# Performance work log

Measured on AMD Instinct MI355X. Metric: run time of the kernel, lower is better.

## Reference

```python
import jax, jax.numpy as jnp
import numpy as np

N_NODES = 100000
N_EDGES = 3200000
N_F = 128
HIDDEN = 128
N_PRED = 8
K_HOPS = 3
N_GRAPHS = 64


def setup_inputs() -> dict:
    key = jax.random.key(0)
    k1, k2, k3, k4, k5, k6, k7, k8 = jax.random.split(key, 8)
    x = jax.random.normal(k1, (N_NODES, N_F), dtype=jnp.float32)
    edge_index = jax.random.randint(k2, (2, N_EDGES), 0, N_NODES, dtype=jnp.int64)
    edge_attr = jax.random.uniform(k3, (N_EDGES,), dtype=jnp.float32)
    batch = jnp.sort(jax.random.randint(k4, (N_NODES,), 0, N_GRAPHS, dtype=jnp.int64))
    # SGConv internal Linear: in=n_f, out=hidden (applied after K propagations)
    s1 = 1.0 / np.sqrt(N_F)
    W_conv = jax.random.uniform(k5, (HIDDEN, N_F), dtype=jnp.float32, minval=-s1, maxval=s1)
    b_conv = jax.random.uniform(k6, (HIDDEN,), dtype=jnp.float32, minval=-s1, maxval=s1)
    s2 = 1.0 / np.sqrt(HIDDEN)
    W_lin = jax.random.uniform(k7, (N_PRED, HIDDEN), dtype=jnp.float32, minval=-s2, maxval=s2)
    b_lin = jax.random.uniform(k8, (N_PRED,), dtype=jnp.float32, minval=-s2, maxval=s2)
    return {"x": x, "edge_index": edge_index, "edge_attr": edge_attr, "batch": batch,
            "W_conv": W_conv, "b_conv": b_conv, "W_lin": W_lin, "b_lin": b_lin}


def _gcn_norm(edge_index, edge_weight, num_nodes):
    # Add self-loops with weight 1 (PyG gcn_norm default), then symmetric normalize.
    loop = jnp.arange(num_nodes, dtype=edge_index.dtype)
    row = jnp.concatenate([edge_index[0], loop])
    col = jnp.concatenate([edge_index[1], loop])
    w = jnp.concatenate([edge_weight, jnp.ones((num_nodes,), dtype=edge_weight.dtype)])
    deg = jax.ops.segment_sum(w, col, num_segments=num_nodes)
    dinv = jnp.where(deg > 0, jax.lax.rsqrt(jnp.where(deg > 0, deg, 1.0)), 0.0)
    norm = dinv[row] * w * dinv[col]
    return row, col, norm


def reference(x, edge_index, edge_attr, batch, W_conv, b_conv, W_lin, b_lin):
    N = x.shape[0]
    row, col, norm = _gcn_norm(edge_index, edge_attr, N)
    h = x
    for _ in range(K_HOPS):  # K repeated gather-scale-scatter propagations
        h = jax.ops.segment_sum(norm[:, None] * h[row], col, num_segments=N)
    h = h @ W_conv.T + b_conv  # SGConv linear: [N, hidden]
    # global_mean_pool by batch id
    sums = jax.ops.segment_sum(h, batch, num_segments=N_GRAPHS)
    cnt = jax.ops.segment_sum(jnp.ones((N,), dtype=h.dtype), batch, num_segments=N_GRAPHS)
    pooled = sums / jnp.maximum(cnt, 1.0)[:, None]
    # dropout(p=0.5) is identity in eval mode
    return pooled @ W_lin.T + b_lin
```

## Files before the change

kernel.cpp:

```cpp
#include <hip/hip_runtime.h>

#define NN 100000
#define NE 3200000
#define NF 128
#define NH 128
#define NP 8
#define NG 64

#define CS 16000
#define NC 7
#define NW 64
#define ES (NE / NW)

#define PT 64
#define GP 1024

#define SCAN_B 1024
#define SCAN_NBLK 98

__device__ __forceinline__ unsigned short f2bf(float f) {
    unsigned u = __float_as_uint(f);
    return (unsigned short)((u + 0x7fffu + ((u >> 16) & 1u)) >> 16);
}
__device__ __forceinline__ float bf2f(unsigned short b) {
    return __uint_as_float((unsigned)b << 16);
}

__global__ void k_init(float* __restrict__ cnt, float* __restrict__ psum) {
    int i = blockIdx.x * blockDim.x + threadIdx.x;
    if (i < NG) cnt[i] = 0.0f;
    if (i < NG * NH) psum[i] = 0.0f;
}

__global__ __launch_bounds__(256) void k_hist(const int* __restrict__ row,
                                              unsigned* __restrict__ H) {
    __shared__ unsigned hist[CS];
    int w = blockIdx.x % NW, c = blockIdx.x / NW;
    int rbase = c * CS;
    int nb = (rbase + CS <= NN) ? CS : (NN - rbase);
    for (int i = threadIdx.x; i < nb; i += 256) hist[i] = 0u;
    __syncthreads();
    const int4* r4 = (const int4*)(row + (size_t)w * ES);
    for (int i = threadIdx.x; i < ES / 8; i += 256) {
        int4 a = r4[2 * i], b = r4[2 * i + 1];
        int rs[8] = {a.x, a.y, a.z, a.w, b.x, b.y, b.z, b.w};
#pragma unroll
        for (int j = 0; j < 8; ++j) {
            unsigned rr = (unsigned)(rs[j] - rbase);
            if (rr < (unsigned)nb) atomicAdd(&hist[rr], 1u);
        }
    }
    __syncthreads();
    for (int i = threadIdx.x; i < nb; i += 256) H[(size_t)w * NN + rbase + i] = hist[i];
}

__global__ __launch_bounds__(256) void k_deg_hist(const int* __restrict__ col,
                                                  const float* __restrict__ wt,
                                                  float* __restrict__ Hd) {
    __shared__ float dh[CS];
    int w = blockIdx.x % NW, c = blockIdx.x / NW;
    int rbase = c * CS;
    int nb = (rbase + CS <= NN) ? CS : (NN - rbase);
    for (int i = threadIdx.x; i < nb; i += 256) dh[i] = 0.0f;
    __syncthreads();
    const int4*   c4 = (const int4*)(col + (size_t)w * ES);
    const float4* w4 = (const float4*)(wt + (size_t)w * ES);
    for (int i = threadIdx.x; i < ES / 8; i += 256) {
        int4 a = c4[2 * i], b = c4[2 * i + 1];
        float4 wa = w4[2 * i], wb = w4[2 * i + 1];
        int cc[8] = {a.x, a.y, a.z, a.w, b.x, b.y, b.z, b.w};
        float ww[8] = {wa.x, wa.y, wa.z, wa.w, wb.x, wb.y, wb.z, wb.w};
#pragma unroll
        for (int j = 0; j < 8; ++j) {
            unsigned rr = (unsigned)(cc[j] - rbase);
            if (rr < (unsigned)nb) atomicAdd(&dh[rr], ww[j]);
        }
    }
    __syncthreads();
    for (int i = threadIdx.x; i < nb; i += 256) Hd[(size_t)w * NN + rbase + i] = dh[i];
}

__global__ void k_cnt(const int* __restrict__ batch, float* __restrict__ cnt) {
    __shared__ float c[NG];
    int t = threadIdx.x;
    if (t < NG) c[t] = 0.0f;
    __syncthreads();
    int i = blockIdx.x * blockDim.x + t;
    if (i < NN) atomicAdd(&c[batch[i]], 1.0f);
    __syncthreads();
    if (t < NG && c[t] != 0.0f) atomicAdd(&cnt[t], c[t]);
}

__global__ void k_reduce(const unsigned* __restrict__ H, const float* __restrict__ Hd,
                         int* __restrict__ rcnt, float* __restrict__ dinv) {
    int r = blockIdx.x * blockDim.x + threadIdx.x;
    if (r >= NN) return;
    unsigned s = 0;
    float d = 1.0f;
#pragma unroll
    for (int w = 0; w < NW; ++w) {
        s += H[(size_t)w * NN + r];
        d += Hd[(size_t)w * NN + r];
    }
    rcnt[r] = (int)s;
    dinv[r] = rsqrtf(d);
}

__global__ __launch_bounds__(SCAN_B) void k_scan1(const int* __restrict__ rcnt,
                                                  int* __restrict__ px,
                                                  int* __restrict__ bsum) {
    __shared__ int s[SCAN_B];
    int t = threadIdx.x;
    int i = blockIdx.x * SCAN_B + t;
    int v = (i < NN) ? rcnt[i] : 0;
    s[t] = v;
    __syncthreads();
    for (int off = 1; off < SCAN_B; off <<= 1) {
        int x = (t >= off) ? s[t - off] : 0;
        __syncthreads();
        s[t] += x;
        __syncthreads();
    }
    px[i] = s[t] - v;
    if (t == SCAN_B - 1) bsum[blockIdx.x] = s[t];
}

__global__ void k_scan2(const int* __restrict__ bsum, int* __restrict__ bofs) {
    if (threadIdx.x == 0) {
        int acc = 0;
        for (int b = 0; b < SCAN_NBLK; ++b) { bofs[b] = acc; acc += bsum[b]; }
    }
}

__global__ void k_scan3(const int* __restrict__ px, const int* __restrict__ bofs,
                        int* __restrict__ rowptr) {
    int i = blockIdx.x * blockDim.x + threadIdx.x;
    if (i > NN) return;
    rowptr[i] = px[i] + bofs[i >> 10];
}

__global__ void k_base(const int* __restrict__ rowptr, unsigned* __restrict__ H) {
    int r = blockIdx.x * blockDim.x + threadIdx.x;
    if (r >= NN) return;
    unsigned acc = (unsigned)rowptr[r];
#pragma unroll
    for (int w = 0; w < NW; ++w) {
        unsigned v = H[(size_t)w * NN + r];
        H[(size_t)w * NN + r] = acc;
        acc += v;
    }
}

__global__ __launch_bounds__(256) void k_sort(const int* __restrict__ row,
                                              const int* __restrict__ col,
                                              const float* __restrict__ wt,
                                              const unsigned* __restrict__ B,
                                              const float* __restrict__ dinv,
                                              float2* __restrict__ pack) {
    __shared__ unsigned basel[CS];
    int w = blockIdx.x % NW, c = blockIdx.x / NW;
    int rbase = c * CS;
    int nb = (rbase + CS <= NN) ? CS : (NN - rbase);
    for (int i = threadIdx.x; i < nb; i += 256)
        basel[i] = B[(size_t)w * NN + rbase + i];
    __syncthreads();
    const int4*   r4 = (const int4*)(row + (size_t)w * ES);
    const int4*   c4 = (const int4*)(col + (size_t)w * ES);
    const float4* w4 = (const float4*)(wt + (size_t)w * ES);
    for (int i = threadIdx.x; i < ES / 8; i += 256) {
        int4 ra = r4[2 * i], rb = r4[2 * i + 1];
        int4 ca = c4[2 * i], cb = c4[2 * i + 1];
        float4 wa = w4[2 * i], wb = w4[2 * i + 1];
        int rs[8] = {ra.x, ra.y, ra.z, ra.w, rb.x, rb.y, rb.z, rb.w};
        int cs[8] = {ca.x, ca.y, ca.z, ca.w, cb.x, cb.y, cb.z, cb.w};
        float ww[8] = {wa.x, wa.y, wa.z, wa.w, wb.x, wb.y, wb.z, wb.w};
#pragma unroll
        for (int j = 0; j < 8; ++j) {
            unsigned rr = (unsigned)(rs[j] - rbase);
            if (rr < (unsigned)nb) {
                unsigned pos = atomicAdd(&basel[rr], 1u);
                pack[pos] = make_float2(__int_as_float(cs[j]),
                                        dinv[rs[j]] * ww[j] * dinv[cs[j]]);
            }
        }
    }
}

__global__ void k_q1_gather(const int* __restrict__ rowptr, const float2* __restrict__ pack,
                            const int* __restrict__ batch, const float* __restrict__ dinv,
                            unsigned short* __restrict__ Q) {
    int wid = (blockIdx.x * blockDim.x + threadIdx.x) >> 6;
    int lane = threadIdx.x & 63;
    if (wid >= NN) return;
    int beg = rowptr[wid], end = rowptr[wid + 1];
    float d = dinv[wid];
    float acc = (batch[wid] == lane) ? d * d : 0.0f;
    int e = beg;
    for (; e + 8 <= end; e += 8) {
        float2 p[8];
#pragma unroll
        for (int j = 0; j < 8; ++j) p[j] = pack[e + j];
        int b[8];
#pragma unroll
        for (int j = 0; j < 8; ++j) b[j] = batch[__float_as_int(p[j].x)];
#pragma unroll
        for (int j = 0; j < 8; ++j) acc += (b[j] == lane) ? p[j].y : 0.0f;
    }
    for (; e < end; ++e) {
        float2 p = pack[e];
        acc += (batch[__float_as_int(p.x)] == lane) ? p.y : 0.0f;
    }
    Q[(wid << 6) + lane] = f2bf(acc);
}

__global__ void k_hop_gather(const int* __restrict__ rowptr, const float2* __restrict__ pack,
                             const float* __restrict__ dinv,
                             const unsigned short* __restrict__ Qin,
                             unsigned short* __restrict__ Qout) {
    int wid = (blockIdx.x * blockDim.x + threadIdx.x) >> 6;
    int lane = threadIdx.x & 63;
    if (wid >= NN) return;
    int beg = rowptr[wid], end = rowptr[wid + 1];
    float d = dinv[wid];
    float acc = d * d * bf2f(Qin[(wid << 6) + lane]);
    int e = beg;
    for (; e + 8 <= end; e += 8) {
        float2 p[8];
#pragma unroll
        for (int j = 0; j < 8; ++j) p[j] = pack[e + j];
        unsigned short q[8];
#pragma unroll
        for (int j = 0; j < 8; ++j) q[j] = Qin[(__float_as_int(p[j].x) << 6) + lane];
#pragma unroll
        for (int j = 0; j < 8; ++j) acc += p[j].y * bf2f(q[j]);
    }
    for (; e < end; ++e) {
        float2 p = pack[e];
        acc += p.y * bf2f(Qin[(__float_as_int(p.x) << 6) + lane]);
    }
    Qout[(wid << 6) + lane] = f2bf(acc);
}

__global__ __launch_bounds__(256) void k_pool(const unsigned short* __restrict__ Q,
                                              const float* __restrict__ x,
                                              float* __restrict__ partial) {
    __shared__ unsigned short qsh[PT * NG];
    __shared__ float xs[PT * NF];
    int t = threadIdx.x;
    int f4 = (t & 31) << 2;
    int g0 = (t >> 5) << 3;
    float4 acc[8];
#pragma unroll
    for (int i = 0; i < 8; ++i) acc[i] = make_float4(0.f, 0.f, 0.f, 0.f);

    const int NT = (NN + PT - 1) / PT;
    for (int tile = blockIdx.x; tile < NT; tile += GP) {
        int n0 = tile * PT;
        int nt = min(PT, NN - n0);
        const uint4*  Q4 = (const uint4*)(Q + (size_t)n0 * NG);
        const float4* X4 = (const float4*)(x + (size_t)n0 * NF);
        uint4*  qs4 = (uint4*)qsh;
        float4* xs4 = (float4*)xs;
        for (int i = t; i < nt * (NG / 8); i += 256) qs4[i] = Q4[i];
        for (int i = t; i < nt * (NF / 4); i += 256) xs4[i] = X4[i];
        __syncthreads();
        for (int n = 0; n < nt; ++n) {
            float4 xv = *(const float4*)&xs[n * NF + f4];
            uint4 qu = *(const uint4*)&qsh[n * NG + g0];
            float qv[8];
            qv[0] = __uint_as_float(qu.x << 16);
            qv[1] = __uint_as_float(qu.x & 0xffff0000u);
            qv[2] = __uint_as_float(qu.y << 16);
            qv[3] = __uint_as_float(qu.y & 0xffff0000u);
            qv[4] = __uint_as_float(qu.z << 16);
            qv[5] = __uint_as_float(qu.z & 0xffff0000u);
            qv[6] = __uint_as_float(qu.w << 16);
            qv[7] = __uint_as_float(qu.w & 0xffff0000u);
#pragma unroll
            for (int i = 0; i < 8; ++i) {
                acc[i].x += qv[i] * xv.x;
                acc[i].y += qv[i] * xv.y;
                acc[i].z += qv[i] * xv.z;
                acc[i].w += qv[i] * xv.w;
            }
        }
        __syncthreads();
    }
    float* pb = partial + (size_t)blockIdx.x * (NG * NF);
#pragma unroll
    for (int i = 0; i < 8; ++i)
        *(float4*)&pb[(g0 + i) * NF + f4] = acc[i];
}

__global__ void k_red(const float* __restrict__ partial, float* __restrict__ psum) {
    int gid = blockIdx.x * blockDim.x + threadIdx.x;
    int idx = gid & (NG * NF - 1);
    int j = gid >> 13;
    float acc = 0.0f;
    for (int b = j; b < GP; b += 8)
        acc += partial[(size_t)b * (NG * NF) + idx];
    atomicAdd(&psum[idx], acc);
}

__global__ void k_final(const float* __restrict__ psum, const float* __restrict__ cnt,
                        const float* __restrict__ Wc, const float* __restrict__ bc,
                        const float* __restrict__ Wl, const float* __restrict__ bl,
                        float* __restrict__ out) {
    __shared__ float M[NP * NH];
    __shared__ float bias[NP];
    int t = threadIdx.x;
    for (int idx = t; idx < NP * NH; idx += 256) {
        int p = idx >> 7, f = idx & 127;
        float s = 0.0f;
        for (int h = 0; h < NH; ++h) s += Wl[p * NH + h] * Wc[h * NF + f];
        M[idx] = s;
    }
    if (t < NP) {
        float s = bl[t];
        for (int h = 0; h < NH; ++h) s += Wl[t * NH + h] * bc[h];
        bias[t] = s;
    }
    __syncthreads();
    for (int idx = t; idx < NG * NP; idx += 256) {
        int g = idx >> 3, p = idx & 7;
        float inv = 1.0f / fmaxf(cnt[g], 1.0f);
        float s = 0.0f;
        for (int f = 0; f < NF; ++f) s += psum[g * NF + f] * M[p * NH + f];
        out[idx] = s * inv + bias[p];
    }
}

extern "C" void kernel_launch(void* const* d_in, const int* in_sizes, int n_in,
                              void* d_out, int out_size, void* d_ws, size_t ws_size,
                              hipStream_t stream) {
    const float* x     = (const float*)d_in[0];
    const int*   ei    = (const int*)d_in[1];
    const float* ea    = (const float*)d_in[2];
    const int*   batch = (const int*)d_in[3];
    const float* Wc    = (const float*)d_in[4];
    const float* bc    = (const float*)d_in[5];
    const float* Wl    = (const float*)d_in[6];
    const float* bl    = (const float*)d_in[7];
    const int* row = ei;
    const int* col = ei + NE;
    float* out = (float*)d_out;

    float* ws     = (float*)d_ws;
    float*  dinv   = ws;
    int*    rowptr = (int*)(dinv + NN);
    float*  cnt    = (float*)(rowptr + NN + 4);
    float*  psum   = cnt + NG;
    float2* pack   = (float2*)(psum + NG * NH);
    unsigned* H    = (unsigned*)(pack + NE);
    float*    Hd   = (float*)(H + (size_t)NW * NN);
    unsigned short* Qa = (unsigned short*)H;
    unsigned short* Qb = Qa + (size_t)NN * NG;
    float* partial = (float*)Qb;
    int* rcnt = (int*)pack;
    int* px   = rcnt + SCAN_NBLK * SCAN_B;
    int* bsum = px + SCAN_NBLK * SCAN_B;
    int* bofs = bsum + SCAN_NBLK;

    const int B = 256;
    int gN  = (NN + B - 1) / B;
    int gCW = NC * NW;
    int gW  = (int)(((long long)NN * 64 + B - 1) / B);

    k_init<<<(NG * NH + B - 1) / B, B, 0, stream>>>(cnt, psum);
    k_hist<<<gCW, B, 0, stream>>>(row, H);
    k_deg_hist<<<gCW, B, 0, stream>>>(col, ea, Hd);
    k_cnt<<<gN, B, 0, stream>>>(batch, cnt);
    k_reduce<<<gN, B, 0, stream>>>(H, Hd, rcnt, dinv);

    k_scan1<<<SCAN_NBLK, SCAN_B, 0, stream>>>(rcnt, px, bsum);
    k_scan2<<<1, 64, 0, stream>>>(bsum, bofs);
    k_scan3<<<(NN + 1 + SCAN_B - 1) / SCAN_B, SCAN_B, 0, stream>>>(px, bofs, rowptr);
    k_base<<<gN, B, 0, stream>>>(rowptr, H);
    k_sort<<<gCW, B, 0, stream>>>(row, col, ea, H, dinv, pack);

    k_q1_gather<<<gW, B, 0, stream>>>(rowptr, pack, batch, dinv, Qa);
    k_hop_gather<<<gW, B, 0, stream>>>(rowptr, pack, dinv, Qa, Qb);
    k_hop_gather<<<gW, B, 0, stream>>>(rowptr, pack, dinv, Qb, Qa);

    k_pool<<<GP, B, 0, stream>>>(Qa, x, partial);
    k_red<<<256, B, 0, stream>>>(partial, psum);
    k_final<<<1, B, 0, stream>>>(psum, cnt, Wc, bc, Wl, bl, out);
}
```

Before: 685.8 us.

## Split each wavefront into 8 edge slots with 16-byte bf16 row loads

The gather kernels now split each 64-lane wavefront into 8 edge slots of 8 lanes. Each lane loads a uint4 holding 8 bf16 values of the 64-wide Q row, so each pass handles 8 edges at once. A one-step prefetch of the packed edge data overlaps the next edge load with the current gather. Partial sums are combined with xor shuffles and written as a vectorized uint4 store. This is meant to raise memory-level parallelism and cut per-edge instruction and latency cost, in exchange for more registers and the shuffle reduction.

```diff
diff --git a/kernel.cpp b/kernel.cpp
--- a/kernel.cpp
+++ b/kernel.cpp
@@ -192,25 +192,44 @@
     int wid = (blockIdx.x * blockDim.x + threadIdx.x) >> 6;
     int lane = threadIdx.x & 63;
     if (wid >= NN) return;
+    int es = lane >> 3;
+    int gg = lane & 7;
     int beg = rowptr[wid], end = rowptr[wid + 1];
     float d = dinv[wid];
-    float acc = (batch[wid] == lane) ? d * d : 0.0f;
-    int e = beg;
-    for (; e + 8 <= end; e += 8) {
-        float2 p[8];
-#pragma unroll
-        for (int j = 0; j < 8; ++j) p[j] = pack[e + j];
-        int b[8];
-#pragma unroll
-        for (int j = 0; j < 8; ++j) b[j] = batch[__float_as_int(p[j].x)];
-#pragma unroll
-        for (int j = 0; j < 8; ++j) acc += (b[j] == lane) ? p[j].y : 0.0f;
-    }
-    for (; e < end; ++e) {
-        float2 p = pack[e];
-        acc += (batch[__float_as_int(p.x)] == lane) ? p.y : 0.0f;
-    }
-    Q[(wid << 6) + lane] = f2bf(acc);
+    int bself = batch[wid];
+    float dd = d * d;
+    float acc[8];
+#pragma unroll
+    for (int i = 0; i < 8; ++i)
+        acc[i] = (es == 0 && bself == gg * 8 + i) ? dd : 0.0f;
+
+    if (beg < end) {
+        int last = end - 1;
+        int idx0 = beg + es; if (idx0 > last) idx0 = last;
+        float2 pe = pack[idx0];
+        for (int e = beg; e < end; e += 8) {
+            int nidx = e + 8 + es; if (nidx > last) nidx = last;
+            float2 pnext = pack[nidx];
+            int   cc = __float_as_int(pe.x);
+            float w  = (e + es <= last) ? pe.y : 0.0f;
+            int b = batch[cc];
+#pragma unroll
+            for (int i = 0; i < 8; ++i) acc[i] += (b == gg * 8 + i) ? w : 0.0f;
+            pe = pnext;
+        }
+    }
+#pragma unroll
+    for (int m = 8; m <= 32; m <<= 1)
+#pragma unroll
+        for (int i = 0; i < 8; ++i) acc[i] += __shfl_xor(acc[i], m, 64);
+    if (es == 0) {
+        uint4 o;
+        o.x = (unsigned)f2bf(acc[0]) | ((unsigned)f2bf(acc[1]) << 16);
+        o.y = (unsigned)f2bf(acc[2]) | ((unsigned)f2bf(acc[3]) << 16);
+        o.z = (unsigned)f2bf(acc[4]) | ((unsigned)f2bf(acc[5]) << 16);
+        o.w = (unsigned)f2bf(acc[6]) | ((unsigned)f2bf(acc[7]) << 16);
+        ((uint4*)Q)[(size_t)wid * 8 + gg] = o;
+    }
 }
 
 __global__ void k_hop_gather(const int* __restrict__ rowptr, const float2* __restrict__ pack,
@@ -220,25 +239,62 @@
     int wid = (blockIdx.x * blockDim.x + threadIdx.x) >> 6;
     int lane = threadIdx.x & 63;
     if (wid >= NN) return;
+    int es = lane >> 3;
+    int gg = lane & 7;
     int beg = rowptr[wid], end = rowptr[wid + 1];
     float d = dinv[wid];
-    float acc = d * d * bf2f(Qin[(wid << 6) + lane]);
-    int e = beg;
-    for (; e + 8 <= end; e += 8) {
-        float2 p[8];
-#pragma unroll
-        for (int j = 0; j < 8; ++j) p[j] = pack[e + j];
-        unsigned short q[8];
-#pragma unroll
-        for (int j = 0; j < 8; ++j) q[j] = Qin[(__float_as_int(p[j].x) << 6) + lane];
-#pragma unroll
-        for (int j = 0; j < 8; ++j) acc += p[j].y * bf2f(q[j]);
-    }
-    for (; e < end; ++e) {
-        float2 p = pack[e];
-        acc += p.y * bf2f(Qin[(__float_as_int(p.x) << 6) + lane]);
-    }
-    Qout[(wid << 6) + lane] = f2bf(acc);
+    const uint4* Q4 = (const uint4*)Qin;
+
+    float acc[8];
+    if (es == 0) {
+        uint4 qs = Q4[(size_t)wid * 8 + gg];
+        float dd = d * d;
+        acc[0] = dd * __uint_as_float(qs.x << 16);
+        acc[1] = dd * __uint_as_float(qs.x & 0xffff0000u);
+        acc[2] = dd * __uint_as_float(qs.y << 16);
+        acc[3] = dd * __uint_as_float(qs.y & 0xffff0000u);
+        acc[4] = dd * __uint_as_float(qs.z << 16);
+        acc[5] = dd * __uint_as_float(qs.z & 0xffff0000u);
+        acc[6] = dd * __uint_as_float(qs.w << 16);
+        acc[7] = dd * __uint_as_float(qs.w & 0xffff0000u);
+    } else {
+#pragma unroll
+        for (int i = 0; i < 8; ++i) acc[i] = 0.0f;
+    }
+
+    if (beg < end) {
+        int last = end - 1;
+        int idx0 = beg + es; if (idx0 > last) idx0 = last;
+        float2 pe = pack[idx0];
+        for (int e = beg; e < end; e += 8) {
+            int nidx = e + 8 + es; if (nidx > last) nidx = last;
+            float2 pnext = pack[nidx];
+            int   cc = __float_as_int(pe.x);
+            float w  = (e + es <= last) ? pe.y : 0.0f;
+            uint4 qv = Q4[(size_t)cc * 8 + gg];
+            acc[0] += w * __uint_as_float(qv.x << 16);
+            acc[1] += w * __uint_as_float(qv.x & 0xffff0000u);
+            acc[2] += w * __uint_as_float(qv.y << 16);
+            acc[3] += w * __uint_as_float(qv.y & 0xffff0000u);
+            acc[4] += w * __uint_as_float(qv.z << 16);
+            acc[5] += w * __uint_as_float(qv.z & 0xffff0000u);
+            acc[6] += w * __uint_as_float(qv.w << 16);
+            acc[7] += w * __uint_as_float(qv.w & 0xffff0000u);
+            pe = pnext;
+        }
+    }
+#pragma unroll
+    for (int m = 8; m <= 32; m <<= 1)
+#pragma unroll
+        for (int i = 0; i < 8; ++i) acc[i] += __shfl_xor(acc[i], m, 64);
+    if (es == 0) {
+        uint4 o;
+        o.x = (unsigned)f2bf(acc[0]) | ((unsigned)f2bf(acc[1]) << 16);
+        o.y = (unsigned)f2bf(acc[2]) | ((unsigned)f2bf(acc[3]) << 16);
+        o.z = (unsigned)f2bf(acc[4]) | ((unsigned)f2bf(acc[5]) << 16);
+        o.w = (unsigned)f2bf(acc[6]) | ((unsigned)f2bf(acc[7]) << 16);
+        ((uint4*)Qout)[(size_t)wid * 8 + gg] = o;
+    }
 }
 
 __global__ __launch_bounds__(256) void k_pool(const unsigned short* __restrict__ Q,
```

Result: faster. 615.1 us (-10.3%).
